# Kernel tuning notes

Hardware: AMD Instinct MI355X
Metric: run time of the kernel (lower is better)

Reference implementation:

```python
import jax, jax.numpy as jnp
import numpy as np

B, T, I, H, L, C = 64, 512, 512, 1024, 4, 1000


def _gru_layer(x_seq, Wih, Whh, bih, bhh):
    """Run one GRU layer over the full sequence.
    x_seq: [B, T, In]; Wih: [3H, In]; Whh: [3H, H]; bih, bhh: [3H].
    Returns (outputs [B, T, H], final hidden [B, H]).
    GRUCell math (PyTorch):
      r = sigmoid(Wir x + bir + Whr h + bhr)
      z = sigmoid(Wiz x + biz + Whz h + bhz)
      n = tanh(Win x + bin + r * (Whn h + bhn))
      h' = (1 - z) * n + z * h
    """
    # Precompute all input-side gate projections in one big GEMM: [B,T,3H]
    gx = jnp.einsum('bti,gi->btg', x_seq, Wih) + bih
    gx = jnp.moveaxis(gx, 1, 0)  # [T, B, 3H] for scan
    h0 = jnp.zeros((x_seq.shape[0], Whh.shape[1]), dtype=x_seq.dtype)

    def step(h, gx_t):
        gh = h @ Whh.T + bhh                       # [B, 3H]
        xr, xz, xn = jnp.split(gx_t, 3, axis=-1)
        hr, hz, hn = jnp.split(gh, 3, axis=-1)
        r = jax.nn.sigmoid(xr + hr)
        z = jax.nn.sigmoid(xz + hz)
        n = jnp.tanh(xn + r * hn)
        h_new = (1.0 - z) * n + z * h
        return h_new, h_new

    h_last, ys = jax.lax.scan(step, h0, gx)
    return jnp.moveaxis(ys, 0, 1), h_last


def setup_inputs() -> dict:
    key = jax.random.key(0)
    ks = jax.random.split(key, 2 + 4 * L + 2)
    inp = {"x": jax.random.normal(ks[0], (B, T, I), dtype=jnp.float32)}
    s = 1.0 / np.sqrt(H)  # PyTorch GRUCell init scale
    kidx = 1
    for l in range(L):
        in_dim = I if l == 0 else H
        inp[f"Wih{l}"] = jax.random.uniform(ks[kidx + 0], (3 * H, in_dim), minval=-s, maxval=s, dtype=jnp.float32)
        inp[f"Whh{l}"] = jax.random.uniform(ks[kidx + 1], (3 * H, H), minval=-s, maxval=s, dtype=jnp.float32)
        inp[f"bih{l}"] = jax.random.uniform(ks[kidx + 2], (3 * H,), minval=-s, maxval=s, dtype=jnp.float32)
        inp[f"bhh{l}"] = jax.random.uniform(ks[kidx + 3], (3 * H,), minval=-s, maxval=s, dtype=jnp.float32)
        kidx += 4
    inp["fc_w"] = jax.random.uniform(ks[kidx], (C, H), minval=-s, maxval=s, dtype=jnp.float32)
    inp["fc_b"] = jax.random.uniform(ks[kidx + 1], (C,), minval=-s, maxval=s, dtype=jnp.float32)
    return inp


def reference(x, Wih0, Whh0, bih0, bhh0, Wih1, Whh1, bih1, bhh1,
              Wih2, Whh2, bih2, bhh2, Wih3, Whh3, bih3, bhh3, fc_w, fc_b):
    layers = [(Wih0, Whh0, bih0, bhh0), (Wih1, Whh1, bih1, bhh1),
              (Wih2, Whh2, bih2, bhh2), (Wih3, Whh3, bih3, bhh3)]
    seq = x
    h_last = None
    for Wih, Whh, bih, bhh in layers:
        seq, h_last = _gru_layer(seq, Wih, Whh, bih, bhh)
    return h_last @ fc_w.T + fc_b  # [B, num_classes]
```

## Files before the change

### kernel.cpp

```cpp
#include <hip/hip_runtime.h>

#define B_ 64
#define T_ 512
#define IN0_ 512
#define H_ 1024
#define C_ 1000
#define NWG 256
#define NTHR 256

typedef _Float16 f16;
typedef _Float16 f16x8 __attribute__((ext_vector_type(8)));
typedef _Float16 f16x4 __attribute__((ext_vector_type(4)));
typedef float f32x4 __attribute__((ext_vector_type(4)));

struct Args {
  const float* x;
  const float* Wih[4];
  const float* Whh[4];
  const float* bih[4];
  const float* bhh[4];
  const float* fcw;
  const float* fcb;
  float* out;
  f16* wpack;
  f16* x16;
  f16* hist;
  float* h32f;
  int* flags;
  int* clk;
  int* bar;
  int RM;
};

__device__ __forceinline__ float sigmoid_f(float x) {
  return 1.0f / (1.0f + __expf(-x));
}
__device__ __forceinline__ float tanh_f(float x) {
  return 1.0f - 2.0f / (__expf(2.0f * x) + 1.0f);
}

__device__ __forceinline__ void heavy_barrier(int* bar) {
  __threadfence();
  __syncthreads();
  if (threadIdx.x == 0) {
    int* cnt = bar;
    int* gen = bar + 1;
    int g = __hip_atomic_load(gen, __ATOMIC_RELAXED, __HIP_MEMORY_SCOPE_AGENT);
    int v = __hip_atomic_fetch_add(cnt, 1, __ATOMIC_ACQ_REL, __HIP_MEMORY_SCOPE_AGENT);
    if (v == NWG - 1) {
      __hip_atomic_store(cnt, 0, __ATOMIC_RELAXED, __HIP_MEMORY_SCOPE_AGENT);
      __hip_atomic_store(gen, g + 1, __ATOMIC_RELEASE, __HIP_MEMORY_SCOPE_AGENT);
    } else {
      int cur;
      do {
        __builtin_amdgcn_s_sleep(2);
        cur = __hip_atomic_load(gen, __ATOMIC_ACQUIRE, __HIP_MEMORY_SCOPE_AGENT);
      } while (cur == g);
    }
  }
  __syncthreads();
  __threadfence();
}

__device__ __forceinline__ void astore8(f16* p, unsigned long long v) {
  __hip_atomic_store((unsigned long long*)p, v, __ATOMIC_RELAXED,
                     __HIP_MEMORY_SCOPE_AGENT);
}
union UF32 { float f; unsigned u; };
__device__ __forceinline__ void astore4(float* p, float v) {
  UF32 c; c.f = v;
  __hip_atomic_store((unsigned*)p, c.u, __ATOMIC_RELAXED,
                     __HIP_MEMORY_SCOPE_AGENT);
}

__device__ __forceinline__ int fload(const int* f) {
  return __hip_atomic_load(f, __ATOMIC_RELAXED, __HIP_MEMORY_SCOPE_AGENT);
}
__device__ __forceinline__ void fstore(int* f, int v) {
  __hip_atomic_store(f, v, __ATOMIC_RELAXED, __HIP_MEMORY_SCOPE_AGENT);
}

__constant__ __device__ const size_t WOFF_[4] = {0ul, 4718592ul, 11010048ul, 17301504ul};

__device__ __forceinline__ int ridx(int bank, int rb, int i, int lane) {
  return ((bank * 4 + rb) * 4 + i) * 64 + lane;
}

template <int IN, bool XA>
__device__ void run_layer(const Args& a, int layer, int sub, bool is_last,
                          float* red, float* hlds, f16* hstage) {
  constexpr int NKB = (IN + H_) / 32;
  constexpr int NXB = IN / 32;
  constexpr int SLICE = NKB / 4;
  constexpr int HSTART = (IN == IN0_) ? 1 : 2;

  const int tid = threadIdx.x;
  const int wave = tid >> 6;
  const int lane = tid & 63;
  const int jc = lane & 15;
  const int kg = lane >> 4;
  const int j = sub * 16 + jc;
  const int wbase = wave * SLICE;
  const int fid = layer * 64 + sub;
  const int RM = a.RM;

  const float bir = a.bih[layer][j], bhr = a.bhh[layer][j];
  const float biz = a.bih[layer][H_ + j], bhz = a.bhh[layer][H_ + j];
  const float bin_ = a.bih[layer][2 * H_ + j], bhn = a.bhh[layer][2 * H_ + j];

  const f16x8* wpb = (const f16x8*)(a.wpack + WOFF_[layer] +
                                    (size_t)sub * 3 * NKB * 512) + lane;
  f16x8 wfR[SLICE], wfZ[SLICE], wfN[SLICE];
#pragma unroll
  for (int kk = 0; kk < SLICE; ++kk) {
    wfR[kk] = wpb[(size_t)(0 * NKB + wbase + kk) * 64];
    wfZ[kk] = wpb[(size_t)(1 * NKB + wbase + kk) * 64];
    wfN[kk] = wpb[(size_t)(2 * NKB + wbase + kk) * 64];
  }

  f16* hring = a.hist + (size_t)layer * RM * B_ * H_;
  const f16* xring = XA ? a.hist + (size_t)(layer - 1) * RM * B_ * H_
                        : (const f16*)nullptr;

  for (int t = 0; t < T_; ++t) {
    if (sub == 0) {
      if (wave >= HSTART) {
        if (t >= 1) {
          const int* f = a.flags + (layer * 64 + lane) * 32;
          while (fload(f) < t) __builtin_amdgcn_s_sleep(1);
        }
        if (wave == HSTART && lane == 0)
          fstore(a.clk + layer * 32, t);
      } else if (XA) {
        if (lane == 0) {
          const int* c = a.clk + (layer - 1) * 32;
          while (fload(c) < t + 1) __builtin_amdgcn_s_sleep(1);
        }
      }
    } else {
      if (wave >= HSTART) {
        if (t >= 1 && lane == 0) {
          const int* c = a.clk + layer * 32;
          while (fload(c) < t) __builtin_amdgcn_s_sleep(1);
        }
      } else if (XA) {
        if (lane == 0) {
          const int* c = a.clk + (layer - 1) * 32;
          while (fload(c) < t + 1) __builtin_amdgcn_s_sleep(1);
        }
      }
    }
    if (wave == 3 && lane == 1 && layer < 3 && t + 1 >= RM) {
      const int* c = a.clk + (layer + 1) * 32;
      while (fload(c) < t + 2 - RM) __builtin_amdgcn_s_sleep(1);
    }

    const f16* xbase = XA ? (xring + (size_t)((t + 1) % RM) * B_ * H_)
                          : (a.x16 + (size_t)t * B_ * IN0_);
    const f16* hbase = hring + (size_t)(t % RM) * B_ * H_;
    f16* ho = hring + (size_t)((t + 1) % RM) * B_ * H_;

    f32x4 aR[4], aZ[4], aNX[4], aNH[4];
#pragma unroll
    for (int rb = 0; rb < 4; ++rb) {
      aR[rb] = 0.f; aZ[rb] = 0.f; aNX[rb] = 0.f; aNH[rb] = 0.f;
    }

#define LOADRB(BUF, RB)                                                      \
  do {                                                                       \
    const int arow_ = (RB) * 16 + jc;                                        \
    const f16* xrow_ = xbase + (size_t)arow_ * IN + kg * 8;                  \
    const f16* hrow_ = hbase + (size_t)arow_ * H_ + kg * 8;                  \
    _Pragma("unroll")                                                        \
    for (int kk = 0; kk < SLICE; ++kk) {                                     \
      const int kb_ = wbase + kk;                                            \
      BUF[kk] = (kb_ < NXB) ? *(const f16x8*)(xrow_ + kb_ * 32)              \
                            : *(const f16x8*)(hrow_ + (kb_ - NXB) * 32);     \
    }                                                                        \
  } while (0)

#define MFMARB(BUF, RB)                                                      \
  do {                                                                       \
    _Pragma("unroll")                                                        \
    for (int kk = 0; kk < SLICE; ++kk) {                                     \
      const int kb_ = wbase + kk;                                            \
      const bool isx_ = kb_ < NXB;                                           \
      const f16x8 af_ = BUF[kk];                                             \
      aR[RB] = __builtin_amdgcn_mfma_f32_16x16x32_f16(af_, wfR[kk], aR[RB], 0, 0, 0); \
      aZ[RB] = __builtin_amdgcn_mfma_f32_16x16x32_f16(af_, wfZ[kk], aZ[RB], 0, 0, 0); \
      const f16x8 z8_ = {0, 0, 0, 0, 0, 0, 0, 0};                            \
      const f16x8 afx_ = isx_ ? af_ : z8_;                                   \
      const f16x8 afh_ = isx_ ? z8_ : af_;                                   \
      aNX[RB] = __builtin_amdgcn_mfma_f32_16x16x32_f16(afx_, wfN[kk], aNX[RB], 0, 0, 0); \
      aNH[RB] = __builtin_amdgcn_mfma_f32_16x16x32_f16(afh_, wfN[kk], aNH[RB], 0, 0, 0); \
    }                                                                        \
  } while (0)

    {
      f16x8 bufA[SLICE], bufB[SLICE];
      LOADRB(bufA, 0);
      LOADRB(bufB, 1);
      MFMARB(bufA, 0);
      LOADRB(bufA, 2);
      MFMARB(bufB, 1);
      LOADRB(bufB, 3);
      MFMARB(bufA, 2);
      MFMARB(bufB, 3);
    }
#undef LOADRB
#undef MFMARB

    if (wave < 2) {
#pragma unroll
      for (int rb = 0; rb < 4; ++rb)
#pragma unroll
        for (int i = 0; i < 4; ++i) {
          red[ridx(0 + wave, rb, i, lane)] = aR[rb][i];
          red[ridx(2 + wave, rb, i, lane)] = aZ[rb][i];
          red[ridx(4 + wave, rb, i, lane)] = aNX[rb][i];
          red[ridx(6 + wave, rb, i, lane)] = aNH[rb][i];
        }
    }
    __syncthreads();
    if (wave >= 2) {
      const int p = wave - 2;
#pragma unroll
      for (int rb = 0; rb < 4; ++rb)
#pragma unroll
        for (int i = 0; i < 4; ++i) {
          red[ridx(0 + p, rb, i, lane)] += aR[rb][i];
          red[ridx(2 + p, rb, i, lane)] += aZ[rb][i];
          red[ridx(4 + p, rb, i, lane)] += aNX[rb][i];
          red[ridx(6 + p, rb, i, lane)] += aNH[rb][i];
        }
    }
    __syncthreads();

    {
#pragma unroll
      for (int i = 0; i < 4; ++i) {
        const int b = wave * 16 + kg * 4 + i;
        const float R  = red[ridx(0, wave, i, lane)] + red[ridx(1, wave, i, lane)];
        const float Z  = red[ridx(2, wave, i, lane)] + red[ridx(3, wave, i, lane)];
        const float NX = red[ridx(4, wave, i, lane)] + red[ridx(5, wave, i, lane)];
        const float NH = red[ridx(6, wave, i, lane)] + red[ridx(7, wave, i, lane)];
        const float r = sigmoid_f(R + bir + bhr);
        const float zz = sigmoid_f(Z + biz + bhz);
        const float nn = tanh_f(NX + bin_ + r * (NH + bhn));
        const float hp = hlds[b * 17 + jc];
        const float hnew = (1.0f - zz) * nn + zz * hp;
        hlds[b * 17 + jc] = hnew;
        hstage[b * 20 + jc] = (f16)hnew;
        if (is_last && t == T_ - 1) astore4(&a.h32f[(size_t)b * H_ + j], hnew);
      }
    }
    __syncthreads();
    {
      const int b = tid >> 2;
      const int c = tid & 3;
      const unsigned long long v =
          *(const unsigned long long*)&hstage[b * 20 + c * 4];
      astore8(&ho[(size_t)b * H_ + sub * 16 + c * 4], v);
    }

    asm volatile("s_waitcnt vmcnt(0) lgkmcnt(0)" ::: "memory");
    __syncthreads();
    if (tid == 0) fstore(a.flags + fid * 32, t + 1);
  }

  if (sub == 0 && layer < 3 && wave == 0) {
    const int* f = a.flags + (layer * 64 + lane) * 32;
    while (fload(f) < T_) __builtin_amdgcn_s_sleep(1);
    if (lane == 0) fstore(a.clk + layer * 32, T_);
  }
}

__global__ void __launch_bounds__(NTHR, 1) gru_pipeline(Args a) {
  __shared__ float red[8 * 4 * 4 * 64];
  __shared__ float hlds[B_ * 17];
  __shared__ f16 hstage[B_ * 20];

  const int tid = threadIdx.x;
  const int gtid = blockIdx.x * NTHR + tid;
  const int NT = NWG * NTHR;

  {
    const int nf4 = B_ * T_ * IN0_ / 4;
    for (int i = gtid; i < nf4; i += NT) {
      int k4 = i & 127;
      int q = i >> 7;
      int b = q & 63;
      int t = q >> 6;
      const float4 v = *(const float4*)(a.x + ((size_t)b * T_ + t) * IN0_ + k4 * 4);
      f16x4 o;
      o[0] = (f16)v.x; o[1] = (f16)v.y; o[2] = (f16)v.z; o[3] = (f16)v.w;
      *(f16x4*)(a.x16 + (size_t)i * 4) = o;
    }
  }
  {
    f16x8 z8 = {0, 0, 0, 0, 0, 0, 0, 0};
    for (int i = gtid; i < 4 * B_ * H_ / 8; i += NT) {
      int l = i / (B_ * H_ / 8);
      int o = i - l * (B_ * H_ / 8);
      ((f16x8*)(a.hist + (size_t)l * a.RM * B_ * H_))[o] = z8;
    }
  }
  for (int i = tid; i < B_ * 17; i += NTHR) hlds[i] = 0.f;
  for (int l = 0; l < 4; ++l) {
    const int In = l ? H_ : IN0_;
    const int K = In + H_;
    const int NKB = K / 32;
    const float* Wih = a.Wih[l];
    const float* Whh = a.Whh[l];
    f16* wp = a.wpack + WOFF_[l];
    const int nunits = 3 * H_ * K / 8;
    for (int uu = gtid; uu < nunits; uu += NT) {
      int lane = uu & 63;
      int q = uu >> 6;
      int kb = q % NKB; q /= NKB;
      int gate = q % 3;
      int subb = q / 3;
      int j = subb * 16 + (lane & 15);
      int g = gate * H_ + j;
      int k = kb * 32 + (lane >> 4) * 8;
      const float* src = (k < In) ? (Wih + (size_t)g * In + k)
                                  : (Whh + (size_t)g * H_ + (k - In));
      f16x8 vv;
#pragma unroll
      for (int e = 0; e < 8; ++e) vv[e] = (f16)src[e];
      ((f16x8*)wp)[uu] = vv;
    }
  }

  heavy_barrier(a.bar);

  const int wg = blockIdx.x;
  const int xslot = wg & 7;
  const int layer = xslot >> 1;
  const int sub = (wg >> 3) * 2 + (xslot & 1);

  if (layer == 0) run_layer<IN0_, false>(a, layer, sub, false, red, hlds, hstage);
  else            run_layer<H_, true>(a, layer, sub, layer == 3, red, hlds, hstage);

  heavy_barrier(a.bar);

  for (int o = gtid; o < B_ * C_; o += NT) {
    const int b = o / C_;
    const int c = o - b * C_;
    const float* hv = a.h32f + (size_t)b * H_;
    const float* wv = a.fcw + (size_t)c * H_;
    float s = a.fcb[c];
    for (int k = 0; k < H_; k += 4) {
      const float4 h4 = *(const float4*)(hv + k);
      const float4 w4 = *(const float4*)(wv + k);
      s = fmaf(h4.x, w4.x, s);
      s = fmaf(h4.y, w4.y, s);
      s = fmaf(h4.z, w4.z, s);
      s = fmaf(h4.w, w4.w, s);
    }
    a.out[o] = s;
  }
}

extern "C" void kernel_launch(void* const* d_in, const int* in_sizes, int n_in,
                              void* d_out, int out_size, void* d_ws, size_t ws_size,
                              hipStream_t stream) {
  Args a;
  a.x = (const float*)d_in[0];
  for (int l = 0; l < 4; ++l) {
    a.Wih[l] = (const float*)d_in[1 + 4 * l];
    a.Whh[l] = (const float*)d_in[2 + 4 * l];
    a.bih[l] = (const float*)d_in[3 + 4 * l];
    a.bhh[l] = (const float*)d_in[4 + 4 * l];
  }
  a.fcw = (const float*)d_in[17];
  a.fcb = (const float*)d_in[18];
  a.out = (float*)d_out;

  const size_t fixed = 23592960ul * 2
                     + 16777216ul * 2
                     + (size_t)B_ * H_ * 4
                     + NWG * 32 * sizeof(int) + 4 * 32 * sizeof(int) + 256;
  const int cand[] = {T_ + 1, 257, 129, 65, 33, 17};
  int RM = 17;
  for (int i = 0; i < 6; ++i) {
    size_t need = fixed + 4ul * cand[i] * B_ * H_ * 2;
    if (need <= ws_size) { RM = cand[i]; break; }
  }
  a.RM = RM;

  char* ws = (char*)d_ws;
  size_t off = 0;
  a.wpack = (f16*)(ws + off); off += 23592960ul * 2;
  a.x16   = (f16*)(ws + off); off += 16777216ul * 2;
  a.hist  = (f16*)(ws + off); off += 4ul * RM * B_ * H_ * 2;
  a.h32f  = (float*)(ws + off); off += (size_t)B_ * H_ * 4;
  a.flags = (int*)(ws + off); off += NWG * 32 * sizeof(int);
  a.clk   = (int*)(ws + off); off += 4 * 32 * sizeof(int);
  a.bar   = (int*)(ws + off); off += 256;

  hipMemsetAsync(a.flags, 0,
                 NWG * 32 * sizeof(int) + 4 * 32 * sizeof(int) + 256, stream);

  void* params[] = { &a };
  hipError_t err = hipLaunchCooperativeKernel((void*)gru_pipeline, dim3(NWG),
                                              dim3(NTHR), params, 0, stream);
  if (err != hipSuccess) {
    gru_pipeline<<<dim3(NWG), dim3(NTHR), 0, stream>>>(a);
  }
}
```

Baseline: 7.777 ms.

## Split GRU K-reduction across eight waves per workgroup with specialized MFMA paths

Doubles threads per workgroup from 256 to 512 so each wave handles half as many K-blocks of the fused input+hidden GEMV. Waves whose slice is purely input or purely hidden skip the unused N-gate MFMA, so they issue three MFMAs per block instead of four. The cross-wave LDS reduction gains two more stages and two more barriers. Hidden-state stores are narrowed to 32-bit to match the thread count. The cost is more synchronization per timestep and a higher register/LDS demand per workgroup, with launch_bounds no longer pinned at one block per CU.

```diff
diff --git a/kernel.cpp b/kernel.cpp
--- a/kernel.cpp
+++ b/kernel.cpp
@@ -6,7 +6,7 @@
 #define H_ 1024
 #define C_ 1000
 #define NWG 256
-#define NTHR 256
+#define NTHR 512
 
 typedef _Float16 f16;
 typedef _Float16 f16x8 __attribute__((ext_vector_type(8)));
@@ -62,9 +62,8 @@
   __threadfence();
 }
 
-__device__ __forceinline__ void astore8(f16* p, unsigned long long v) {
-  __hip_atomic_store((unsigned long long*)p, v, __ATOMIC_RELAXED,
-                     __HIP_MEMORY_SCOPE_AGENT);
+__device__ __forceinline__ void astoreu32(unsigned* p, unsigned v) {
+  __hip_atomic_store(p, v, __ATOMIC_RELAXED, __HIP_MEMORY_SCOPE_AGENT);
 }
 union UF32 { float f; unsigned u; };
 __device__ __forceinline__ void astore4(float* p, float v) {
@@ -72,7 +71,6 @@
   __hip_atomic_store((unsigned*)p, c.u, __ATOMIC_RELAXED,
                      __HIP_MEMORY_SCOPE_AGENT);
 }
-
 __device__ __forceinline__ int fload(const int* f) {
   return __hip_atomic_load(f, __ATOMIC_RELAXED, __HIP_MEMORY_SCOPE_AGENT);
 }
@@ -82,8 +80,8 @@
 
 __constant__ __device__ const size_t WOFF_[4] = {0ul, 4718592ul, 11010048ul, 17301504ul};
 
-__device__ __forceinline__ int ridx(int bank, int rb, int i, int lane) {
-  return ((bank * 4 + rb) * 4 + i) * 64 + lane;
+__device__ __forceinline__ int ridx2(int q, int s, int rb, int i, int lane) {
+  return (((q * 2 + s) * 4 + rb) * 4 + i) * 64 + lane;
 }
 
 template <int IN, bool XA>
@@ -91,8 +89,8 @@
                           float* red, float* hlds, f16* hstage) {
   constexpr int NKB = (IN + H_) / 32;
   constexpr int NXB = IN / 32;
-  constexpr int SLICE = NKB / 4;
-  constexpr int HSTART = (IN == IN0_) ? 1 : 2;
+  constexpr int SLICE = NKB / 8;
+  constexpr int HSTART = NXB / SLICE;
 
   const int tid = threadIdx.x;
   const int wave = tid >> 6;
@@ -101,6 +99,8 @@
   const int kg = lane >> 4;
   const int j = sub * 16 + jc;
   const int wbase = wave * SLICE;
+  const bool hasX = (wbase < NXB);
+  const bool hasH = (wbase + SLICE > NXB);
   const int fid = layer * 64 + sub;
   const int RM = a.RM;
 
@@ -108,8 +108,9 @@
   const float biz = a.bih[layer][H_ + j], bhz = a.bhh[layer][H_ + j];
   const float bin_ = a.bih[layer][2 * H_ + j], bhn = a.bhh[layer][2 * H_ + j];
 
-  const f16x8* wpb = (const f16x8*)(a.wpack + WOFF_[layer] +
-                                    (size_t)sub * 3 * NKB * 512) + lane;
+  const volatile f16x8* wpb =
+      (const volatile f16x8*)(a.wpack + WOFF_[layer] +
+                              (size_t)sub * 3 * NKB * 512) + lane;
   f16x8 wfR[SLICE], wfZ[SLICE], wfN[SLICE];
 #pragma unroll
   for (int kk = 0; kk < SLICE; ++kk) {
@@ -124,7 +125,7 @@
 
   for (int t = 0; t < T_; ++t) {
     if (sub == 0) {
-      if (wave >= HSTART) {
+      if (hasH) {
         if (t >= 1) {
           const int* f = a.flags + (layer * 64 + lane) * 32;
           while (fload(f) < t) __builtin_amdgcn_s_sleep(1);
@@ -138,7 +139,7 @@
         }
       }
     } else {
-      if (wave >= HSTART) {
+      if (hasH) {
         if (t >= 1 && lane == 0) {
           const int* c = a.clk + layer * 32;
           while (fload(c) < t) __builtin_amdgcn_s_sleep(1);
@@ -150,7 +151,7 @@
         }
       }
     }
-    if (wave == 3 && lane == 1 && layer < 3 && t + 1 >= RM) {
+    if (wave == 0 && lane == 1 && layer < 3 && t + 1 >= RM) {
       const int* c = a.clk + (layer + 1) * 32;
       while (fload(c) < t + 2 - RM) __builtin_amdgcn_s_sleep(1);
     }
@@ -181,18 +182,36 @@
 
 #define MFMARB(BUF, RB)                                                      \
   do {                                                                       \
-    _Pragma("unroll")                                                        \
-    for (int kk = 0; kk < SLICE; ++kk) {                                     \
-      const int kb_ = wbase + kk;                                            \
-      const bool isx_ = kb_ < NXB;                                           \
-      const f16x8 af_ = BUF[kk];                                             \
-      aR[RB] = __builtin_amdgcn_mfma_f32_16x16x32_f16(af_, wfR[kk], aR[RB], 0, 0, 0); \
-      aZ[RB] = __builtin_amdgcn_mfma_f32_16x16x32_f16(af_, wfZ[kk], aZ[RB], 0, 0, 0); \
-      const f16x8 z8_ = {0, 0, 0, 0, 0, 0, 0, 0};                            \
-      const f16x8 afx_ = isx_ ? af_ : z8_;                                   \
-      const f16x8 afh_ = isx_ ? z8_ : af_;                                   \
-      aNX[RB] = __builtin_amdgcn_mfma_f32_16x16x32_f16(afx_, wfN[kk], aNX[RB], 0, 0, 0); \
-      aNH[RB] = __builtin_amdgcn_mfma_f32_16x16x32_f16(afh_, wfN[kk], aNH[RB], 0, 0, 0); \
+    if (!hasH) {                                                             \
+      _Pragma("unroll")                                                      \
+      for (int kk = 0; kk < SLICE; ++kk) {                                   \
+        const f16x8 af_ = BUF[kk];                                           \
+        aR[RB] = __builtin_amdgcn_mfma_f32_16x16x32_f16(af_, wfR[kk], aR[RB], 0, 0, 0); \
+        aZ[RB] = __builtin_amdgcn_mfma_f32_16x16x32_f16(af_, wfZ[kk], aZ[RB], 0, 0, 0); \
+        aNX[RB] = __builtin_amdgcn_mfma_f32_16x16x32_f16(af_, wfN[kk], aNX[RB], 0, 0, 0); \
+      }                                                                      \
+    } else if (!hasX) {                                                      \
+      _Pragma("unroll")                                                      \
+      for (int kk = 0; kk < SLICE; ++kk) {                                   \
+        const f16x8 af_ = BUF[kk];                                           \
+        aR[RB] = __builtin_amdgcn_mfma_f32_16x16x32_f16(af_, wfR[kk], aR[RB], 0, 0, 0); \
+        aZ[RB] = __builtin_amdgcn_mfma_f32_16x16x32_f16(af_, wfZ[kk], aZ[RB], 0, 0, 0); \
+        aNH[RB] = __builtin_amdgcn_mfma_f32_16x16x32_f16(af_, wfN[kk], aNH[RB], 0, 0, 0); \
+      }                                                                      \
+    } else {                                                                 \
+      _Pragma("unroll")                                                      \
+      for (int kk = 0; kk < SLICE; ++kk) {                                   \
+        const int kb_ = wbase + kk;                                          \
+        const bool isx_ = kb_ < NXB;                                         \
+        const f16x8 af_ = BUF[kk];                                           \
+        aR[RB] = __builtin_amdgcn_mfma_f32_16x16x32_f16(af_, wfR[kk], aR[RB], 0, 0, 0); \
+        aZ[RB] = __builtin_amdgcn_mfma_f32_16x16x32_f16(af_, wfZ[kk], aZ[RB], 0, 0, 0); \
+        const f16x8 z8_ = {0, 0, 0, 0, 0, 0, 0, 0};                          \
+        const f16x8 afx_ = isx_ ? af_ : z8_;                                 \
+        const f16x8 afh_ = isx_ ? z8_ : af_;                                 \
+        aNX[RB] = __builtin_amdgcn_mfma_f32_16x16x32_f16(afx_, wfN[kk], aNX[RB], 0, 0, 0); \
+        aNH[RB] = __builtin_amdgcn_mfma_f32_16x16x32_f16(afh_, wfN[kk], aNH[RB], 0, 0, 0); \
+      }                                                                      \
     }                                                                        \
   } while (0)
 
@@ -215,35 +234,64 @@
       for (int rb = 0; rb < 4; ++rb)
 #pragma unroll
         for (int i = 0; i < 4; ++i) {
-          red[ridx(0 + wave, rb, i, lane)] = aR[rb][i];
-          red[ridx(2 + wave, rb, i, lane)] = aZ[rb][i];
-          red[ridx(4 + wave, rb, i, lane)] = aNX[rb][i];
-          red[ridx(6 + wave, rb, i, lane)] = aNH[rb][i];
-        }
-    }
-    __syncthreads();
-    if (wave >= 2) {
-      const int p = wave - 2;
+          red[ridx2(0, wave, rb, i, lane)] = aR[rb][i];
+          red[ridx2(1, wave, rb, i, lane)] = aZ[rb][i];
+          red[ridx2(2, wave, rb, i, lane)] = hasX ? aNX[rb][i] : 0.f;
+          red[ridx2(3, wave, rb, i, lane)] = hasH ? aNH[rb][i] : 0.f;
+        }
+    }
+    __syncthreads();
+    if (wave == 2 || wave == 3) {
+      const int s = wave - 2;
 #pragma unroll
       for (int rb = 0; rb < 4; ++rb)
 #pragma unroll
         for (int i = 0; i < 4; ++i) {
-          red[ridx(0 + p, rb, i, lane)] += aR[rb][i];
-          red[ridx(2 + p, rb, i, lane)] += aZ[rb][i];
-          red[ridx(4 + p, rb, i, lane)] += aNX[rb][i];
-          red[ridx(6 + p, rb, i, lane)] += aNH[rb][i];
+          red[ridx2(0, s, rb, i, lane)] += aR[rb][i];
+          red[ridx2(1, s, rb, i, lane)] += aZ[rb][i];
+          if (hasX) red[ridx2(2, s, rb, i, lane)] += aNX[rb][i];
+          if (hasH) red[ridx2(3, s, rb, i, lane)] += aNH[rb][i];
+        }
+    }
+    __syncthreads();
+    if (wave == 4 || wave == 5) {
+      const int s = wave - 4;
+#pragma unroll
+      for (int rb = 0; rb < 4; ++rb)
+#pragma unroll
+        for (int i = 0; i < 4; ++i) {
+          red[ridx2(0, s, rb, i, lane)] += aR[rb][i];
+          red[ridx2(1, s, rb, i, lane)] += aZ[rb][i];
+          if (hasX) red[ridx2(2, s, rb, i, lane)] += aNX[rb][i];
+          if (hasH) red[ridx2(3, s, rb, i, lane)] += aNH[rb][i];
+        }
+    }
+    __syncthreads();
+    if (wave == 6 || wave == 7) {
+      const int s = wave - 6;
+#pragma unroll
+      for (int rb = 0; rb < 4; ++rb)
+#pragma unroll
+        for (int i = 0; i < 4; ++i) {
+          red[ridx2(0, s, rb, i, lane)] += aR[rb][i];
+          red[ridx2(1, s, rb, i, lane)] += aZ[rb][i];
+          if (hasX) red[ridx2(2, s, rb, i, lane)] += aNX[rb][i];
+          if (hasH) red[ridx2(3, s, rb, i, lane)] += aNH[rb][i];
         }
     }
     __syncthreads();
 
     {
-#pragma unroll
-      for (int i = 0; i < 4; ++i) {
-        const int b = wave * 16 + kg * 4 + i;
-        const float R  = red[ridx(0, wave, i, lane)] + red[ridx(1, wave, i, lane)];
-        const float Z  = red[ridx(2, wave, i, lane)] + red[ridx(3, wave, i, lane)];
-        const float NX = red[ridx(4, wave, i, lane)] + red[ridx(5, wave, i, lane)];
-        const float NH = red[ridx(6, wave, i, lane)] + red[ridx(7, wave, i, lane)];
+      const int rb = wave >> 1;
+      const int ib = (wave & 1) * 2;
+#pragma unroll
+      for (int ii = 0; ii < 2; ++ii) {
+        const int i = ib + ii;
+        const int b = rb * 16 + kg * 4 + i;
+        const float R  = red[ridx2(0, 0, rb, i, lane)] + red[ridx2(0, 1, rb, i, lane)];
+        const float Z  = red[ridx2(1, 0, rb, i, lane)] + red[ridx2(1, 1, rb, i, lane)];
+        const float NX = red[ridx2(2, 0, rb, i, lane)] + red[ridx2(2, 1, rb, i, lane)];
+        const float NH = red[ridx2(3, 0, rb, i, lane)] + red[ridx2(3, 1, rb, i, lane)];
         const float r = sigmoid_f(R + bir + bhr);
         const float zz = sigmoid_f(Z + biz + bhz);
         const float nn = tanh_f(NX + bin_ + r * (NH + bhn));
@@ -256,11 +304,10 @@
     }
     __syncthreads();
     {
-      const int b = tid >> 2;
-      const int c = tid & 3;
-      const unsigned long long v =
-          *(const unsigned long long*)&hstage[b * 20 + c * 4];
-      astore8(&ho[(size_t)b * H_ + sub * 16 + c * 4], v);
+      const int b = tid >> 3;
+      const int c = tid & 7;
+      const unsigned v = *(const unsigned*)&hstage[b * 20 + c * 2];
+      astoreu32((unsigned*)&ho[(size_t)b * H_ + sub * 16 + c * 2], v);
     }
 
     asm volatile("s_waitcnt vmcnt(0) lgkmcnt(0)" ::: "memory");
@@ -275,8 +322,8 @@
   }
 }
 
-__global__ void __launch_bounds__(NTHR, 1) gru_pipeline(Args a) {
-  __shared__ float red[8 * 4 * 4 * 64];
+__global__ void __launch_bounds__(NTHR) gru_pipeline(Args a) {
+  __shared__ float red[4 * 2 * 4 * 4 * 64];
   __shared__ float hlds[B_ * 17];
   __shared__ f16 hstage[B_ * 20];
 
```

Measured after the change: 7.693 ms. No clear change (-1.1%).
